# Kernel optimization log

Hardware: AMD Instinct MI355X
Metric: run time of the kernel (lower is better)

The kernel has to match this reference:

```python
import jax, jax.numpy as jnp
import numpy as np

B, T, D = 8, 2048, 1024
E, S = 8, 1            # num_experts, num_slots
FF = 4 * (S * D)       # ffn_mult * (num_slots * hiddens)

def setup_inputs() -> dict:
    key = jax.random.key(0)
    ks = jax.random.split(key, 7)
    sd = S * D
    inp = {
        "X":  jax.random.normal(ks[0], (B, T, D), dtype=jnp.float32),
        # slots gating MLP (single linear D -> E*S)
        "Wg": jax.random.normal(ks[1], (D, E * S), dtype=jnp.float32) / np.sqrt(D),
        "bg": jnp.zeros((E * S,), dtype=jnp.float32),
        # expert FFN (weights SHARED across experts, as in source [FFN(...)]*E)
        "W1": jax.random.normal(ks[2], (sd, FF), dtype=jnp.float32) / np.sqrt(sd),
        "b1": jnp.zeros((FF,), dtype=jnp.float32),
        "W2": jax.random.normal(ks[3], (FF, sd), dtype=jnp.float32) / np.sqrt(FF),
        "b2": jnp.zeros((sd,), dtype=jnp.float32),
    }
    return inp

def reference(X, Wg, bg, W1, b1, W2, b2):
    # logits: (B, T, E*S)
    logits = jnp.einsum('btd,de->bte', X, Wg) + bg
    dispatch_w = jax.nn.softmax(logits, axis=1)   # over tokens T
    combine_w = jax.nn.softmax(logits, axis=2)    # over slots E*S
    # slots = dispatch_w^T @ X : (B, E*S, D) -> (B, E, S*D)
    slots = jnp.einsum('bte,btd->bed', dispatch_w, X).reshape(B, E, S * D)
    # shared-weight FFN applied per expert slot (dropout=0 at eval)
    h = jax.nn.silu(jnp.einsum('bef,fh->beh', slots, W1) + b1)
    y = jnp.einsum('beh,hf->bef', h, W2) + b2     # (B, E, S*D)
    y = y.reshape(B, E * S, D)
    # combine: (B, T, E*S) @ (B, E*S, D)
    return jnp.einsum('bte,bed->btd', combine_w, y)
```

## Files before the change

kernel.cpp:

```cpp
#include <hip/hip_runtime.h>
#include <math.h>

#define B_  8
#define T_  2048
#define D_  1024
#define E_  8
#define FF_ 4096
#define N_  64
#define BT_ (B_*T_)
#define WGS 1028

__global__ __launch_bounds__(256) void k_logits(
    const float* __restrict__ X, const float* __restrict__ Wg,
    const float* __restrict__ bg, float* __restrict__ logits,
    float* __restrict__ sumexp)
{
    __shared__ float wgT[E_ * WGS];
    __shared__ float xt[32 * 132];
    __shared__ float red[256];

    const int tid = threadIdx.x;

    #pragma unroll
    for (int r = 0; r < 32; ++r) {
        int idx = r * 256 + tid;
        wgT[(idx & 7) * WGS + (idx >> 3)] = Wg[idx];
    }

    const int bt0 = blockIdx.x * 32;
    const int tok = tid >> 3;
    const int e   = tid & 7;
    float acc = 0.f;

    for (int dt = 0; dt < 8; ++dt) {
        __syncthreads();
        #pragma unroll
        for (int r = 0; r < 4; ++r) {
            int idx4 = r * 256 + tid;
            int row = idx4 >> 5, c4 = idx4 & 31;
            const float4 v = *(const float4*)&X[(size_t)(bt0 + row) * D_ + dt * 128 + c4 * 4];
            *(float4*)&xt[row * 132 + c4 * 4] = v;
        }
        __syncthreads();
        const float4* xp = (const float4*)&xt[tok * 132];
        const float4* wp = (const float4*)&wgT[e * WGS + dt * 128];
        #pragma unroll
        for (int j = 0; j < 32; ++j) {
            const float4 xv = xp[j];
            const float4 wv = wp[j];
            acc += xv.x * wv.x + xv.y * wv.y + xv.z * wv.z + xv.w * wv.w;
        }
    }

    const float lg = acc + bg[e];
    logits[(size_t)(bt0 + tok) * E_ + e] = lg;

    red[tid] = expf(lg);
    __syncthreads();
    for (int s = 128; s >= 8; s >>= 1) {
        if (tid < s) red[tid] += red[tid + s];
        __syncthreads();
    }
    if (tid < 8) {
        atomicAdd(&sumexp[(bt0 >> 11) * E_ + tid], red[tid]);
    }
}

__global__ __launch_bounds__(256) void k_slots_part(
    const float* __restrict__ X, const float* __restrict__ logits,
    const float* __restrict__ sumexp, float* __restrict__ part)
{
    __shared__ float wlds[64 * 8];
    __shared__ float inv[8];

    const int tid = threadIdx.x;
    const int ts = blockIdx.x, b = blockIdx.y;
    const int t0 = ts * 64;

    if (tid < 8) inv[tid] = 1.f / sumexp[b * E_ + tid];
    __syncthreads();
    #pragma unroll
    for (int r = 0; r < 2; ++r) {
        int idx = r * 256 + tid;
        wlds[idx] = expf(logits[(size_t)b * T_ * E_ + (size_t)t0 * E_ + idx]) * inv[idx & 7];
    }
    __syncthreads();

    float4 acc[8];
    #pragma unroll
    for (int e = 0; e < 8; ++e) { acc[e].x = acc[e].y = acc[e].z = acc[e].w = 0.f; }

    const float* xb = &X[((size_t)b * T_ + t0) * D_ + tid * 4];
    #pragma unroll 4
    for (int t = 0; t < 64; ++t) {
        const float4 x4 = *(const float4*)&xb[(size_t)t * D_];
        const float4 wA = *(const float4*)&wlds[t * 8];
        const float4 wB = *(const float4*)&wlds[t * 8 + 4];
        const float w[8] = {wA.x, wA.y, wA.z, wA.w, wB.x, wB.y, wB.z, wB.w};
        #pragma unroll
        for (int e = 0; e < 8; ++e) {
            acc[e].x += x4.x * w[e];
            acc[e].y += x4.y * w[e];
            acc[e].z += x4.z * w[e];
            acc[e].w += x4.w * w[e];
        }
    }
    #pragma unroll
    for (int e = 0; e < 8; ++e) {
        *(float4*)&part[(size_t)ts * (N_ * D_) + (size_t)(b * E_ + e) * D_ + tid * 4] = acc[e];
    }
}

__global__ __launch_bounds__(256) void k_reduce_slots(
    const float* __restrict__ part, float* __restrict__ slots)
{
    const int i = blockIdx.x * 256 + threadIdx.x;
    float s = 0.f;
    #pragma unroll
    for (int p = 0; p < 32; ++p) s += part[(size_t)p * (N_ * D_) + i];
    slots[i] = s;
}

__global__ __launch_bounds__(256) void k_gemm_part(
    const float* __restrict__ A, const float* __restrict__ W,
    float* __restrict__ part, int K, int F)
{
    __shared__ float sT[32 * 68];

    const int tid = threadIdx.x;
    const int f0 = blockIdx.x * 512 + tid;
    const int k0 = blockIdx.y * 32;

    #pragma unroll
    for (int r = 0; r < 8; ++r) {
        int idx = r * 256 + tid;
        int n = idx >> 5, kk = idx & 31;
        sT[kk * 68 + n] = A[(size_t)n * K + k0 + kk];
    }
    __syncthreads();

    float acc0[64], acc1[64];
    #pragma unroll
    for (int n = 0; n < 64; ++n) { acc0[n] = 0.f; acc1[n] = 0.f; }

    #pragma unroll 4
    for (int kk = 0; kk < 32; ++kk) {
        const float w0 = W[(size_t)(k0 + kk) * F + f0];
        const float w1 = W[(size_t)(k0 + kk) * F + f0 + 256];
        const float4* sp = (const float4*)&sT[kk * 68];
        #pragma unroll
        for (int j = 0; j < 16; ++j) {
            const float4 s = sp[j];
            acc0[4*j+0] += s.x * w0; acc0[4*j+1] += s.y * w0;
            acc0[4*j+2] += s.z * w0; acc0[4*j+3] += s.w * w0;
            acc1[4*j+0] += s.x * w1; acc1[4*j+1] += s.y * w1;
            acc1[4*j+2] += s.z * w1; acc1[4*j+3] += s.w * w1;
        }
    }

    const size_t base = (size_t)blockIdx.y * N_ * F;
    #pragma unroll
    for (int n = 0; n < 64; ++n) {
        part[base + (size_t)n * F + f0]       = acc0[n];
        part[base + (size_t)n * F + f0 + 256] = acc1[n];
    }
}

__global__ __launch_bounds__(256) void k_reduce_silu(
    const float* __restrict__ part, const float* __restrict__ b1,
    float* __restrict__ h)
{
    const int i = blockIdx.x * 256 + threadIdx.x;
    float s = 0.f;
    #pragma unroll
    for (int p = 0; p < 32; ++p) s += part[(size_t)p * (N_ * FF_) + i];
    s += b1[i & (FF_ - 1)];
    h[i] = s / (1.f + expf(-s));
}

__global__ __launch_bounds__(256) void k_reduce_bias(
    const float* __restrict__ part, const float* __restrict__ b2,
    float* __restrict__ y)
{
    const int i = blockIdx.x * 256 + threadIdx.x;
    float s = 0.f;
    #pragma unroll
    for (int p = 0; p < 128; ++p) s += part[(size_t)p * (N_ * D_) + i];
    y[i] = s + b2[i & (D_ - 1)];
}

__global__ __launch_bounds__(256) void k_combine(
    const float* __restrict__ logits, const float* __restrict__ y,
    float* __restrict__ out)
{
    __shared__ float wlds[64 * 8];
    const int tid = threadIdx.x;
    const int dc = blockIdx.x, tc = blockIdx.y, b = blockIdx.z;
    const int t0 = tc * 64;

    if (tid < 64) {
        const float* lp = &logits[((size_t)b * T_ + t0 + tid) * E_];
        float ex[8]; float s = 0.f;
        #pragma unroll
        for (int i = 0; i < 8; ++i) { ex[i] = expf(lp[i]); s += ex[i]; }
        const float invs = 1.f / s;
        #pragma unroll
        for (int i = 0; i < 8; ++i) wlds[tid * 8 + i] = ex[i] * invs;
    }
    __syncthreads();

    const int d = dc * 256 + tid;
    float yv[8];
    #pragma unroll
    for (int e = 0; e < 8; ++e) yv[e] = y[(size_t)(b * E_ + e) * D_ + d];

    for (int t = 0; t < 64; ++t) {
        const float4 wA = *(const float4*)&wlds[t * 8];
        const float4 wB = *(const float4*)&wlds[t * 8 + 4];
        const float acc = wA.x * yv[0] + wA.y * yv[1] + wA.z * yv[2] + wA.w * yv[3]
                        + wB.x * yv[4] + wB.y * yv[5] + wB.z * yv[6] + wB.w * yv[7];
        out[((size_t)b * T_ + t0 + t) * D_ + d] = acc;
    }
}

extern "C" void kernel_launch(void* const* d_in, const int* in_sizes, int n_in,
                              void* d_out, int out_size, void* d_ws, size_t ws_size,
                              hipStream_t stream)
{
    const float* X  = (const float*)d_in[0];
    const float* Wg = (const float*)d_in[1];
    const float* bg = (const float*)d_in[2];
    const float* W1 = (const float*)d_in[3];
    const float* b1 = (const float*)d_in[4];
    const float* W2 = (const float*)d_in[5];
    const float* b2 = (const float*)d_in[6];
    float* out = (float*)d_out;

    float* wsf    = (float*)d_ws;
    float* logits = wsf;
    float* sumexp = logits + BT_ * E_;
    float* slots  = sumexp + 64;
    float* h      = slots + N_ * D_;
    float* y      = h + N_ * FF_;

    float* part = out;

    hipMemsetAsync(sumexp, 0, 64 * sizeof(float), stream);

    hipLaunchKernelGGL(k_logits,       dim3(BT_ / 32), dim3(256), 0, stream,
                       X, Wg, bg, logits, sumexp);
    hipLaunchKernelGGL(k_slots_part,   dim3(32, 8),    dim3(256), 0, stream,
                       X, logits, sumexp, part);
    hipLaunchKernelGGL(k_reduce_slots, dim3(256),      dim3(256), 0, stream,
                       part, slots);
    hipLaunchKernelGGL(k_gemm_part,    dim3(FF_ / 512, 1024 / 32), dim3(256), 0, stream,
                       slots, W1, part, 1024, FF_);
    hipLaunchKernelGGL(k_reduce_silu,  dim3(N_ * FF_ / 256), dim3(256), 0, stream,
                       part, b1, h);
    hipLaunchKernelGGL(k_gemm_part,    dim3(D_ / 512, FF_ / 32), dim3(256), 0, stream,
                       h, W2, part, FF_, D_);
    hipLaunchKernelGGL(k_reduce_bias,  dim3(N_ * D_ / 256), dim3(256), 0, stream,
                       part, b2, y);
    hipLaunchKernelGGL(k_combine,      dim3(4, 32, 8), dim3(256), 0, stream,
                       logits, y, out);
}
```

Baseline: 272.1 us.

## Split logits over D with merge kernel and retile slot and FFN GEMMs

```diff
diff --git a/kernel.cpp b/kernel.cpp
--- a/kernel.cpp
+++ b/kernel.cpp
@@ -8,81 +8,109 @@
 #define FF_ 4096
 #define N_  64
 #define BT_ (B_*T_)
-#define WGS 1028
-
-__global__ __launch_bounds__(256) void k_logits(
+
+__global__ __launch_bounds__(256) void k_logits_part(
     const float* __restrict__ X, const float* __restrict__ Wg,
-    const float* __restrict__ bg, float* __restrict__ logits,
-    float* __restrict__ sumexp)
-{
-    __shared__ float wgT[E_ * WGS];
-    __shared__ float xt[32 * 132];
-    __shared__ float red[256];
-
-    const int tid = threadIdx.x;
-
-    #pragma unroll
-    for (int r = 0; r < 32; ++r) {
+    float* __restrict__ part)
+{
+    __shared__ float wgT[E_ * 128];
+    __shared__ float xt[256 * 36];
+
+    const int tid = threadIdx.x;
+    const int bt0 = blockIdx.x * 256;
+    const int d0  = blockIdx.y * 128;
+
+    #pragma unroll
+    for (int r = 0; r < 4; ++r) {
         int idx = r * 256 + tid;
-        wgT[(idx & 7) * WGS + (idx >> 3)] = Wg[idx];
-    }
-
-    const int bt0 = blockIdx.x * 32;
-    const int tok = tid >> 3;
-    const int e   = tid & 7;
-    float acc = 0.f;
-
-    for (int dt = 0; dt < 8; ++dt) {
+        wgT[(idx & 7) * 128 + (idx >> 3)] = Wg[(size_t)d0 * E_ + idx];
+    }
+
+    float acc[8];
+    #pragma unroll
+    for (int e = 0; e < 8; ++e) acc[e] = 0.f;
+
+    for (int dt = 0; dt < 4; ++dt) {
         __syncthreads();
         #pragma unroll
-        for (int r = 0; r < 4; ++r) {
-            int idx4 = r * 256 + tid;
-            int row = idx4 >> 5, c4 = idx4 & 31;
-            const float4 v = *(const float4*)&X[(size_t)(bt0 + row) * D_ + dt * 128 + c4 * 4];
-            *(float4*)&xt[row * 132 + c4 * 4] = v;
+        for (int r = 0; r < 8; ++r) {
+            int fi = r * 256 + tid;
+            int token = fi >> 3, dj = fi & 7;
+            const float4 v = *(const float4*)
+                &X[(size_t)(bt0 + token) * D_ + d0 + dt * 32 + dj * 4];
+            *(float4*)&xt[token * 36 + dj * 4] = v;
         }
         __syncthreads();
-        const float4* xp = (const float4*)&xt[tok * 132];
-        const float4* wp = (const float4*)&wgT[e * WGS + dt * 128];
-        #pragma unroll
-        for (int j = 0; j < 32; ++j) {
-            const float4 xv = xp[j];
-            const float4 wv = wp[j];
-            acc += xv.x * wv.x + xv.y * wv.y + xv.z * wv.z + xv.w * wv.w;
-        }
-    }
-
-    const float lg = acc + bg[e];
-    logits[(size_t)(bt0 + tok) * E_ + e] = lg;
-
-    red[tid] = expf(lg);
-    __syncthreads();
-    for (int s = 128; s >= 8; s >>= 1) {
-        if (tid < s) red[tid] += red[tid + s];
+        #pragma unroll
+        for (int dj = 0; dj < 8; ++dj) {
+            const float4 x4 = *(const float4*)&xt[tid * 36 + dj * 4];
+            #pragma unroll
+            for (int e = 0; e < 8; ++e) {
+                const float4 w4 = *(const float4*)&wgT[e * 128 + dt * 32 + dj * 4];
+                acc[e] += x4.x * w4.x + x4.y * w4.y + x4.z * w4.z + x4.w * w4.w;
+            }
+        }
+    }
+
+    float* pp = &part[(size_t)blockIdx.y * BT_ * E_ + (size_t)(bt0 + tid) * E_];
+    *(float4*)&pp[0] = make_float4(acc[0], acc[1], acc[2], acc[3]);
+    *(float4*)&pp[4] = make_float4(acc[4], acc[5], acc[6], acc[7]);
+}
+
+__global__ __launch_bounds__(256) void k_logits_merge(
+    const float* __restrict__ part, const float* __restrict__ bg,
+    float* __restrict__ logits, float* __restrict__ sumexp)
+{
+    __shared__ float red[8 * 256];
+    const int tid = threadIdx.x;
+    const int token = blockIdx.x * 256 + tid;
+    const int b = blockIdx.x >> 3;
+
+    float a[8];
+    #pragma unroll
+    for (int e = 0; e < 8; ++e) a[e] = 0.f;
+    #pragma unroll
+    for (int p = 0; p < 8; ++p) {
+        const float* pp = &part[(size_t)p * BT_ * E_ + (size_t)token * E_];
+        const float4 v0 = *(const float4*)&pp[0];
+        const float4 v1 = *(const float4*)&pp[4];
+        a[0] += v0.x; a[1] += v0.y; a[2] += v0.z; a[3] += v0.w;
+        a[4] += v1.x; a[5] += v1.y; a[6] += v1.z; a[7] += v1.w;
+    }
+    #pragma unroll
+    for (int e = 0; e < 8; ++e) a[e] += bg[e];
+
+    float* lp = &logits[(size_t)token * E_];
+    *(float4*)&lp[0] = make_float4(a[0], a[1], a[2], a[3]);
+    *(float4*)&lp[4] = make_float4(a[4], a[5], a[6], a[7]);
+
+    #pragma unroll
+    for (int e = 0; e < 8; ++e) red[e * 256 + tid] = expf(a[e]);
+    __syncthreads();
+    for (int s = 128; s >= 1; s >>= 1) {
+        if (tid < s) {
+            #pragma unroll
+            for (int e = 0; e < 8; ++e)
+                red[e * 256 + tid] += red[e * 256 + tid + s];
+        }
         __syncthreads();
     }
-    if (tid < 8) {
-        atomicAdd(&sumexp[(bt0 >> 11) * E_ + tid], red[tid]);
-    }
+    if (tid < 8) atomicAdd(&sumexp[b * E_ + tid], red[tid * 256]);
 }
 
 __global__ __launch_bounds__(256) void k_slots_part(
     const float* __restrict__ X, const float* __restrict__ logits,
     const float* __restrict__ sumexp, float* __restrict__ part)
 {
-    __shared__ float wlds[64 * 8];
-    __shared__ float inv[8];
-
+    __shared__ float wlds[32 * 8];
     const int tid = threadIdx.x;
     const int ts = blockIdx.x, b = blockIdx.y;
-    const int t0 = ts * 64;
-
-    if (tid < 8) inv[tid] = 1.f / sumexp[b * E_ + tid];
-    __syncthreads();
-    #pragma unroll
-    for (int r = 0; r < 2; ++r) {
-        int idx = r * 256 + tid;
-        wlds[idx] = expf(logits[(size_t)b * T_ * E_ + (size_t)t0 * E_ + idx]) * inv[idx & 7];
+    const int t0 = ts * 32;
+
+    {
+        int t = tid >> 3, e = tid & 7;
+        wlds[tid] = expf(logits[((size_t)b * T_ + t0 + t) * E_ + e])
+                    / sumexp[b * E_ + e];
     }
     __syncthreads();
 
@@ -91,8 +119,8 @@
     for (int e = 0; e < 8; ++e) { acc[e].x = acc[e].y = acc[e].z = acc[e].w = 0.f; }
 
     const float* xb = &X[((size_t)b * T_ + t0) * D_ + tid * 4];
-    #pragma unroll 4
-    for (int t = 0; t < 64; ++t) {
+    #pragma unroll 8
+    for (int t = 0; t < 32; ++t) {
         const float4 x4 = *(const float4*)&xb[(size_t)t * D_];
         const float4 wA = *(const float4*)&wlds[t * 8];
         const float4 wB = *(const float4*)&wlds[t * 8 + 4];
@@ -117,7 +145,7 @@
     const int i = blockIdx.x * 256 + threadIdx.x;
     float s = 0.f;
     #pragma unroll
-    for (int p = 0; p < 32; ++p) s += part[(size_t)p * (N_ * D_) + i];
+    for (int p = 0; p < 64; ++p) s += part[(size_t)p * (N_ * D_) + i];
     slots[i] = s;
 }
 
@@ -125,45 +153,40 @@
     const float* __restrict__ A, const float* __restrict__ W,
     float* __restrict__ part, int K, int F)
 {
-    __shared__ float sT[32 * 68];
-
-    const int tid = threadIdx.x;
-    const int f0 = blockIdx.x * 512 + tid;
-    const int k0 = blockIdx.y * 32;
-
-    #pragma unroll
-    for (int r = 0; r < 8; ++r) {
+    __shared__ float sT[64 * 68];
+
+    const int tid = threadIdx.x;
+    const int f0 = blockIdx.x * 256 + tid;
+    const int k0 = blockIdx.y * 64;
+
+    #pragma unroll
+    for (int r = 0; r < 16; ++r) {
         int idx = r * 256 + tid;
-        int n = idx >> 5, kk = idx & 31;
+        int n = idx >> 6, kk = idx & 63;
         sT[kk * 68 + n] = A[(size_t)n * K + k0 + kk];
     }
     __syncthreads();
 
-    float acc0[64], acc1[64];
-    #pragma unroll
-    for (int n = 0; n < 64; ++n) { acc0[n] = 0.f; acc1[n] = 0.f; }
+    float acc[64];
+    #pragma unroll
+    for (int n = 0; n < 64; ++n) acc[n] = 0.f;
 
     #pragma unroll 4
-    for (int kk = 0; kk < 32; ++kk) {
-        const float w0 = W[(size_t)(k0 + kk) * F + f0];
-        const float w1 = W[(size_t)(k0 + kk) * F + f0 + 256];
+    for (int kk = 0; kk < 64; ++kk) {
+        const float w = W[(size_t)(k0 + kk) * F + f0];
         const float4* sp = (const float4*)&sT[kk * 68];
         #pragma unroll
         for (int j = 0; j < 16; ++j) {
             const float4 s = sp[j];
-            acc0[4*j+0] += s.x * w0; acc0[4*j+1] += s.y * w0;
-            acc0[4*j+2] += s.z * w0; acc0[4*j+3] += s.w * w0;
-            acc1[4*j+0] += s.x * w1; acc1[4*j+1] += s.y * w1;
-            acc1[4*j+2] += s.z * w1; acc1[4*j+3] += s.w * w1;
+            acc[4*j+0] += s.x * w; acc[4*j+1] += s.y * w;
+            acc[4*j+2] += s.z * w; acc[4*j+3] += s.w * w;
         }
     }
 
     const size_t base = (size_t)blockIdx.y * N_ * F;
     #pragma unroll
-    for (int n = 0; n < 64; ++n) {
-        part[base + (size_t)n * F + f0]       = acc0[n];
-        part[base + (size_t)n * F + f0 + 256] = acc1[n];
-    }
+    for (int n = 0; n < 64; ++n)
+        part[base + (size_t)n * F + f0] = acc[n];
 }
 
 __global__ __launch_bounds__(256) void k_reduce_silu(
@@ -173,7 +196,7 @@
     const int i = blockIdx.x * 256 + threadIdx.x;
     float s = 0.f;
     #pragma unroll
-    for (int p = 0; p < 32; ++p) s += part[(size_t)p * (N_ * FF_) + i];
+    for (int p = 0; p < 16; ++p) s += part[(size_t)p * (N_ * FF_) + i];
     s += b1[i & (FF_ - 1)];
     h[i] = s / (1.f + expf(-s));
 }
@@ -185,7 +208,7 @@
     const int i = blockIdx.x * 256 + threadIdx.x;
     float s = 0.f;
     #pragma unroll
-    for (int p = 0; p < 128; ++p) s += part[(size_t)p * (N_ * D_) + i];
+    for (int p = 0; p < 64; ++p) s += part[(size_t)p * (N_ * D_) + i];
     y[i] = s + b2[i & (D_ - 1)];
 }
 
@@ -247,17 +270,19 @@
 
     hipMemsetAsync(sumexp, 0, 64 * sizeof(float), stream);
 
-    hipLaunchKernelGGL(k_logits,       dim3(BT_ / 32), dim3(256), 0, stream,
-                       X, Wg, bg, logits, sumexp);
-    hipLaunchKernelGGL(k_slots_part,   dim3(32, 8),    dim3(256), 0, stream,
+    hipLaunchKernelGGL(k_logits_part,  dim3(BT_ / 256, 8), dim3(256), 0, stream,
+                       X, Wg, part);
+    hipLaunchKernelGGL(k_logits_merge, dim3(BT_ / 256),    dim3(256), 0, stream,
+                       part, bg, logits, sumexp);
+    hipLaunchKernelGGL(k_slots_part,   dim3(64, 8),        dim3(256), 0, stream,
                        X, logits, sumexp, part);
-    hipLaunchKernelGGL(k_reduce_slots, dim3(256),      dim3(256), 0, stream,
+    hipLaunchKernelGGL(k_reduce_slots, dim3(256),          dim3(256), 0, stream,
                        part, slots);
-    hipLaunchKernelGGL(k_gemm_part,    dim3(FF_ / 512, 1024 / 32), dim3(256), 0, stream,
+    hipLaunchKernelGGL(k_gemm_part,    dim3(FF_ / 256, 1024 / 64), dim3(256), 0, stream,
                        slots, W1, part, 1024, FF_);
     hipLaunchKernelGGL(k_reduce_silu,  dim3(N_ * FF_ / 256), dim3(256), 0, stream,
                        part, b1, h);
-    hipLaunchKernelGGL(k_gemm_part,    dim3(D_ / 512, FF_ / 32), dim3(256), 0, stream,
+    hipLaunchKernelGGL(k_gemm_part,    dim3(D_ / 256, FF_ / 64), dim3(256), 0, stream,
                        h, W2, part, FF_, D_);
     hipLaunchKernelGGL(k_reduce_bias,  dim3(N_ * D_ / 256), dim3(256), 0, stream,
                        part, b2, y);
```

New measurement: 318.9 us. 17.2% more time.
